# Kernel tuning notes

Hardware: AMD Instinct MI355X
Metric: run time of the kernel (lower is better)

Reference implementation:

```python
import jax, jax.numpy as jnp
import numpy as np

D_MODEL, D_FF, N_EXPERTS, TOP_K = 1024, 4096, 8, 2
BATCH, SEQ = 4, 2048


def setup_inputs() -> dict:
    key = jax.random.key(0)
    ks = jax.random.split(key, 8)
    s_in = 1.0 / np.sqrt(D_MODEL)
    s_ff = 1.0 / np.sqrt(D_FF)
    return {
        "x": jax.random.normal(ks[0], (BATCH, SEQ, D_MODEL), dtype=jnp.float32),
        "W_gate": jax.random.uniform(ks[1], (D_MODEL, N_EXPERTS), jnp.float32, -s_in, s_in),
        "b_gate": jax.random.uniform(ks[2], (N_EXPERTS,), jnp.float32, -s_in, s_in),
        "W1": jax.random.uniform(ks[3], (N_EXPERTS, D_MODEL, D_FF), jnp.float32, -s_in, s_in),
        "b1": jax.random.uniform(ks[4], (N_EXPERTS, D_FF), jnp.float32, -s_in, s_in),
        "W2": jax.random.uniform(ks[5], (N_EXPERTS, D_FF, D_MODEL), jnp.float32, -s_ff, s_ff),
        "b2": jax.random.uniform(ks[6], (N_EXPERTS, D_MODEL), jnp.float32, -s_ff, s_ff),
    }


def reference(x, W_gate, b_gate, W1, b1, W2, b2):
    B, S, D = x.shape
    # Router
    logits = jnp.einsum("bsd,de->bse", x, W_gate) + b_gate           # [B,S,E]
    probs = jax.nn.softmax(logits, axis=-1)
    top_p, top_i = jax.lax.top_k(probs, TOP_K)                        # [B,S,k]
    top_p = top_p / jnp.sum(top_p, axis=-1, keepdims=True)
    
    x_flat = x.reshape(-1, D)                                         # [T,D]
    idx_flat = top_i.reshape(-1, TOP_K)                               # [T,k]
    p_flat = top_p.reshape(-1, TOP_K)                                 # [T,k]
    
    # Dense all-expert FFN (faithful to original: every expert on every token)
    h = jax.nn.relu(jnp.einsum("td,edf->etf", x_flat, W1) + b1[:, None, :])  # [E,T,F]
    expert_out = jnp.einsum("etf,efd->etd", h, W2) + b2[:, None, :]          # [E,T,D]
    expert_out = jnp.transpose(expert_out, (1, 0, 2))                 # [T,E,D]
    
    # Gather top-k expert outputs and combine
    sel = jnp.take_along_axis(expert_out, idx_flat[:, :, None], axis=1)  # [T,k,D]
    out_flat = jnp.sum(sel * p_flat[:, :, None], axis=1)              # [T,D]
    output = out_flat.reshape(B, S, D)
    
    # torch.var defaults to unbiased (ddof=1)
    load_balance_loss = jnp.var(jnp.mean(probs, axis=(0, 1)), ddof=1)
    return (output, load_balance_loss)
```

## Files before the change

kernel.cpp:

```cpp
#include <hip/hip_runtime.h>
#include <cstdint>
#include <cstddef>

#define D_MODEL 1024
#define D_FF    4096
#define NEXP    8
#define NTOK    8192
#define MAXT    136
#define CAP     (MAXT * 128)

typedef unsigned short ushort_t;
typedef __attribute__((ext_vector_type(8))) short   short8;
typedef __attribute__((ext_vector_type(4))) float   floatx4;
typedef __attribute__((ext_vector_type(4))) unsigned short ushort4v;

__device__ __forceinline__ ushort_t f2bf(float f) {
    union { float f; uint32_t u; } v; v.f = f;
    uint32_t r = v.u + 0x7fffu + ((v.u >> 16) & 1u);
    return (ushort_t)(r >> 16);
}

__device__ __forceinline__ floatx4 mfma16(short8 a, short8 b, floatx4 c) {
    return __builtin_amdgcn_mfma_f32_16x16x32_bf16(a, b, c, 0, 0, 0);
}

__device__ __forceinline__ int tile_decode(const int* __restrict__ counts,
                                           int tm, int& e_out, int& row0) {
    int cnts[NEXP];
#pragma unroll
    for (int e = 0; e < NEXP; ++e) cnts[e] = counts[e];
    int b = 0, t = tm;
#pragma unroll
    for (int e = 0; e < NEXP; ++e) {
        int nt = (cnts[e] + 127) >> 7;
        if (t < nt) { e_out = e; row0 = b + t * 128; return 1; }
        t -= nt; b += nt * 128;
    }
    return 0;
}

__global__ __launch_bounds__(256)
void transpose_all(const float* __restrict__ W1, const float* __restrict__ W2,
                   ushort_t* __restrict__ W1T, ushort_t* __restrict__ W2T)
{
    __shared__ float t[64][65];
    int bid = blockIdx.x;
    const float* in; ushort_t* out; int R, C, rt, ct;
    if (bid < 8192) {
        int e = bid >> 10, rem = bid & 1023;
        R = D_MODEL; C = D_FF; rt = rem >> 6; ct = rem & 63;
        in = W1 + (size_t)e * R * C; out = W1T + (size_t)e * R * C;
    } else {
        int e = (bid - 8192) >> 10, rem = bid & 1023;
        R = D_FF; C = D_MODEL; rt = rem >> 4; ct = rem & 15;
        in = W2 + (size_t)e * R * C; out = W2T + (size_t)e * R * C;
    }
    int r0 = rt * 64, c0 = ct * 64, tid = threadIdx.x;
    int lr = tid >> 4, lc4 = (tid & 15) * 4;
#pragma unroll
    for (int p = 0; p < 4; ++p) {
        int rr = p * 16 + lr;
        float4 v = *(const float4*)(in + (size_t)(r0 + rr) * C + c0 + lc4);
        t[rr][lc4] = v.x; t[rr][lc4 + 1] = v.y; t[rr][lc4 + 2] = v.z; t[rr][lc4 + 3] = v.w;
    }
    __syncthreads();
    int orw = tid >> 3, j0 = (tid & 7) * 8;
#pragma unroll
    for (int p = 0; p < 2; ++p) {
        int orow = p * 32 + orw;
        ushort_t pk[8];
#pragma unroll
        for (int i = 0; i < 8; ++i) pk[i] = f2bf(t[j0 + i][orow]);
        *(short8*)(out + (size_t)(c0 + orow) * R + r0 + j0) = *(short8*)pk;
    }
}

__global__ __launch_bounds__(256)
void router_kernel(const float* __restrict__ x, const float* __restrict__ Wg,
                   const float* __restrict__ bg,
                   int* __restrict__ counts, int* __restrict__ slot_tok,
                   float* __restrict__ slot_p, float* __restrict__ psum)
{
    __shared__ float bsum[NEXP];
    int tid = threadIdx.x;
    if (tid < NEXP) bsum[tid] = 0.f;
    __syncthreads();

    int t = (blockIdx.x * 256 + tid) >> 6;
    int l = tid & 63;
    const float* xr = x + (size_t)t * D_MODEL;
    float acc[NEXP] = {0.f,0.f,0.f,0.f,0.f,0.f,0.f,0.f};
#pragma unroll 4
    for (int c = 0; c < D_MODEL / 64; ++c) {
        int d = c * 64 + l;
        float xv = xr[d];
        const float4* wr = (const float4*)(Wg + (size_t)d * NEXP);
        float4 w0 = wr[0], w1 = wr[1];
        acc[0] += xv * w0.x; acc[1] += xv * w0.y;
        acc[2] += xv * w0.z; acc[3] += xv * w0.w;
        acc[4] += xv * w1.x; acc[5] += xv * w1.y;
        acc[6] += xv * w1.z; acc[7] += xv * w1.w;
    }
#pragma unroll
    for (int off = 32; off >= 1; off >>= 1)
#pragma unroll
        for (int e = 0; e < NEXP; ++e)
            acc[e] += __shfl_xor(acc[e], off);

    if (l == 0) {
        float lg[NEXP], mx = -1e30f;
#pragma unroll
        for (int e = 0; e < NEXP; ++e) { lg[e] = acc[e] + bg[e]; mx = fmaxf(mx, lg[e]); }
        float pr[NEXP], s = 0.f;
#pragma unroll
        for (int e = 0; e < NEXP; ++e) { pr[e] = __expf(lg[e] - mx); s += pr[e]; }
        float inv = 1.f / s;
#pragma unroll
        for (int e = 0; e < NEXP; ++e) pr[e] *= inv;
        int e0 = 0;
#pragma unroll
        for (int e = 1; e < NEXP; ++e) if (pr[e] > pr[e0]) e0 = e;
        int e1 = (e0 == 0) ? 1 : 0;
#pragma unroll
        for (int e = 0; e < NEXP; ++e) if (e != e0 && pr[e] > pr[e1]) e1 = e;
        float pnorm = 1.f / (pr[e0] + pr[e1]);
        int s0 = atomicAdd(&counts[e0], 1);
        slot_tok[e0 * NTOK + s0] = t; slot_p[e0 * NTOK + s0] = pr[e0] * pnorm;
        int s1 = atomicAdd(&counts[e1], 1);
        slot_tok[e1 * NTOK + s1] = t; slot_p[e1 * NTOK + s1] = pr[e1] * pnorm;
#pragma unroll
        for (int e = 0; e < NEXP; ++e) atomicAdd(&bsum[e], pr[e]);
    }
    __syncthreads();
    if (tid < NEXP) atomicAdd(&psum[tid], bsum[tid]);
}

__global__ __launch_bounds__(256)
void gather_kernel(const float* __restrict__ x, const int* __restrict__ counts,
                   const int* __restrict__ slot_tok, const float* __restrict__ slot_p,
                   ushort_t* __restrict__ xg, float* __restrict__ tok_prob,
                   int* __restrict__ tcount, int* __restrict__ tok2row)
{
    __shared__ int sb[NEXP + 1];
    int row = blockIdx.x, tid = threadIdx.x;
    if (tid == 0) {
        int b = 0;
#pragma unroll
        for (int e = 0; e < NEXP; ++e) { sb[e] = b; b += ((counts[e] + 127) >> 7) << 7; }
        sb[NEXP] = b;
    }
    __syncthreads();
    if (row >= sb[NEXP]) return;
    int e = 0;
    while (e < NEXP - 1 && row >= sb[e + 1]) ++e;
    int lr = row - sb[e];
    int tok = -1; float pr = 0.f;
    if (lr < counts[e]) { tok = slot_tok[e * NTOK + lr]; pr = slot_p[e * NTOK + lr]; }
    if (tid == 0) {
        tok_prob[row] = pr;
        if (tok >= 0) {
            int s = atomicAdd(&tcount[tok], 1);
            tok2row[tok * 2 + s] = row;
        }
    }
    ushort_t* dst = xg + (size_t)row * D_MODEL;
    if (tok >= 0) {
        float4 v = ((const float4*)(x + (size_t)tok * D_MODEL))[tid];
        ushort4v o; o.x = f2bf(v.x); o.y = f2bf(v.y); o.z = f2bf(v.z); o.w = f2bf(v.w);
        *(ushort4v*)(dst + tid * 4) = o;
    } else {
        *(ushort4v*)(dst + tid * 4) = ushort4v{0, 0, 0, 0};
    }
}

template <int EPI>
__global__ __launch_bounds__(256, 2)
void gemm_tile(const ushort_t* __restrict__ A, const ushort_t* __restrict__ B,
               int K, int N, const int* __restrict__ counts,
               int row_lo, int row_hi,
               ushort_t* __restrict__ Hout, const float* __restrict__ bias,
               float* __restrict__ Yout)
{
    int NX = gridDim.x;
    int lin = blockIdx.y * NX + blockIdx.x;
    int sid = lin >> 4, wi = lin & 15;
    int nsx = NX >> 2;
    int sx = sid % nsx, sy = sid / nsx;
    int colbase = ((sx << 2) + (wi & 3)) * 128;
    int tm = (sy << 2) + (wi >> 2);

    int e, row0;
    if (!tile_decode(counts, tm, e, row0)) return;
    if (row0 < row_lo || row0 >= row_hi) return;

    __shared__ ushort_t smem[128 * 64 * 2];
    ushort_t* As = smem;
    ushort_t* Bs = smem + 128 * 64;

    int tid = threadIdx.x;
    int w = tid >> 6, l = tid & 63;
    int q = l >> 4, ml = l & 15;
    int wm = w >> 1, wn = w & 1;
    int r8 = l >> 3, ch = l & 7;

    const ushort_t* Ab = A + (size_t)row0 * K;
    const ushort_t* Bb = B + ((size_t)e * N + colbase) * K;

    floatx4 acc[4][4];
#pragma unroll
    for (int i = 0; i < 4; ++i)
#pragma unroll
        for (int j = 0; j < 4; ++j) acc[i][j] = floatx4{0.f, 0.f, 0.f, 0.f};

    short8 sa[4], sb[4];
    int rloc[4];
#pragma unroll
    for (int p = 0; p < 4; ++p) rloc[p] = (p * 4 + w) * 8 + r8;

#define GLOAD(k0)                                                          \
    do {                                                                   \
        _Pragma("unroll")                                                  \
        for (int p = 0; p < 4; ++p) {                                      \
            sa[p] = *(const short8*)(Ab + (size_t)rloc[p] * K + (k0) + ch * 8); \
            sb[p] = *(const short8*)(Bb + (size_t)rloc[p] * K + (k0) + ch * 8); \
        }                                                                  \
    } while (0)

    GLOAD(0);
    int nst = K >> 6;
    for (int s = 0; s < nst; ++s) {
#pragma unroll
        for (int p = 0; p < 4; ++p) {
            int r = rloc[p];
            int c = ch ^ r8;
            *(short8*)(As + r * 64 + c * 8) = sa[p];
            *(short8*)(Bs + r * 64 + c * 8) = sb[p];
        }
        __syncthreads();
        if (s + 1 < nst) GLOAD((s + 1) << 6);
#pragma unroll
        for (int kk = 0; kk < 2; ++kk) {
            int cb = kk * 4 + q;
            short8 av[4], bv[4];
#pragma unroll
            for (int mi = 0; mi < 4; ++mi) {
                int m = wm * 64 + mi * 16 + ml;
                av[mi] = *(const short8*)(As + m * 64 + ((cb ^ (m & 7)) * 8));
            }
#pragma unroll
            for (int ni = 0; ni < 4; ++ni) {
                int n = wn * 64 + ni * 16 + ml;
                bv[ni] = *(const short8*)(Bs + n * 64 + ((cb ^ (n & 7)) * 8));
            }
#pragma unroll
            for (int mi = 0; mi < 4; ++mi)
#pragma unroll
                for (int ni = 0; ni < 4; ++ni)
                    acc[mi][ni] = mfma16(av[mi], bv[ni], acc[mi][ni]);
        }
        __syncthreads();
    }
#undef GLOAD

    float bv4[4];
#pragma unroll
    for (int ni = 0; ni < 4; ++ni)
        bv4[ni] = bias[e * N + colbase + wn * 64 + ni * 16 + ml];

    if (EPI == 0) {
        ushort_t* ct = smem;
#pragma unroll
        for (int mi = 0; mi < 4; ++mi)
#pragma unroll
            for (int ni = 0; ni < 4; ++ni)
#pragma unroll
                for (int r = 0; r < 4; ++r) {
                    float v = acc[mi][ni][r] + bv4[ni];
                    v = v > 0.f ? v : 0.f;
                    ct[(wm * 64 + mi * 16 + q * 4 + r) * 128 + wn * 64 + ni * 16 + ml] = f2bf(v);
                }
        __syncthreads();
#pragma unroll
        for (int i = 0; i < 8; ++i) {
            int idx = tid + i * 256;
            int r = idx >> 4, c8 = idx & 15;
            *(short8*)(Hout + (size_t)(row0 + r) * D_FF + colbase + c8 * 8) =
                *(const short8*)(ct + r * 128 + c8 * 8);
        }
    } else {
#pragma unroll
        for (int mi = 0; mi < 4; ++mi)
#pragma unroll
            for (int ni = 0; ni < 4; ++ni)
#pragma unroll
                for (int r = 0; r < 4; ++r) {
                    int row = row0 + wm * 64 + mi * 16 + q * 4 + r;
                    int col = colbase + wn * 64 + ni * 16 + ml;
                    Yout[(size_t)row * N + col] = acc[mi][ni][r] + bv4[ni];
                }
    }
}

__global__ __launch_bounds__(256)
void combine_kernel(const float* __restrict__ y, const int* __restrict__ tok2row,
                    const float* __restrict__ tok_prob, float* __restrict__ out,
                    const float* __restrict__ psum, float* __restrict__ loss_out)
{
    int t = blockIdx.x;
    if (t == 0 && threadIdx.x == 0) {
        float me[NEXP], m = 0.f;
#pragma unroll
        for (int e = 0; e < NEXP; ++e) { me[e] = psum[e] * (1.f / NTOK); m += me[e] * (1.f / NEXP); }
        float v = 0.f;
#pragma unroll
        for (int e = 0; e < NEXP; ++e) v += (me[e] - m) * (me[e] - m);
        loss_out[0] = v * (1.f / (NEXP - 1));
    }
    int r0 = tok2row[t * 2], r1 = tok2row[t * 2 + 1];
    float p0 = tok_prob[r0], p1 = tok_prob[r1];
    int c = threadIdx.x;
    float4 a = ((const float4*)(y + (size_t)r0 * D_MODEL))[c];
    float4 b = ((const float4*)(y + (size_t)r1 * D_MODEL))[c];
    float4 o;
    o.x = p0 * a.x + p1 * b.x;
    o.y = p0 * a.y + p1 * b.y;
    o.z = p0 * a.z + p1 * b.z;
    o.w = p0 * a.w + p1 * b.w;
    ((float4*)(out + (size_t)t * D_MODEL))[c] = o;
}

extern "C" void kernel_launch(void* const* d_in, const int* in_sizes, int n_in,
                              void* d_out, int out_size, void* d_ws, size_t ws_size,
                              hipStream_t stream)
{
    const float* x  = (const float*)d_in[0];
    const float* Wg = (const float*)d_in[1];
    const float* bg = (const float*)d_in[2];
    const float* W1 = (const float*)d_in[3];
    const float* b1 = (const float*)d_in[4];
    const float* W2 = (const float*)d_in[5];
    const float* b2 = (const float*)d_in[6];
    float* out = (float*)d_out;

    char* ws = (char*)d_ws;
    size_t off = 0;
    auto alloc = [&](size_t bytes) -> char* {
        char* p = ws + off;
        off = (off + bytes + 255) & ~(size_t)255;
        return p;
    };
    int*      counts   = (int*)alloc(NEXP * 4);
    float*    psum     = (float*)alloc(NEXP * 4);
    int*      tcount   = (int*)alloc(NTOK * 4);
    size_t zero_bytes = off;
    float*    tok_prob = (float*)alloc(CAP * 4);
    int*      tok2row  = (int*)alloc((size_t)NTOK * 2 * 4);
    int*      slot_tok = (int*)alloc((size_t)NEXP * NTOK * 4);
    float*    slot_p   = (float*)alloc((size_t)NEXP * NTOK * 4);
    ushort_t* xg       = (ushort_t*)alloc((size_t)CAP * D_MODEL * 2);
    ushort_t* W1T      = (ushort_t*)alloc((size_t)NEXP * D_MODEL * D_FF * 2);
    ushort_t* W2T      = (ushort_t*)alloc((size_t)NEXP * D_MODEL * D_FF * 2);
    float*    ybuf     = (float*)alloc((size_t)CAP * D_MODEL * 4);
    size_t fixed = off;
    size_t h_full = (size_t)CAP * D_FF * 2;

    int NC = 1;
    if (ws_size < fixed + h_full) NC = 4;
    if (NC == 4 && ws_size < fixed + h_full / 4) NC = 16;
    if (ws_size < fixed + h_full / NC) return;
    int chunk_rows = CAP / NC;
    ushort_t* hbuf = (ushort_t*)alloc(h_full / NC);

    hipMemsetAsync(d_ws, 0, zero_bytes, stream);

    transpose_all<<<16384, 256, 0, stream>>>(W1, W2, W1T, W2T);
    router_kernel<<<NTOK / 4, 256, 0, stream>>>(x, Wg, bg, counts, slot_tok, slot_p, psum);
    gather_kernel<<<CAP, 256, 0, stream>>>(x, counts, slot_tok, slot_p, xg,
                                           tok_prob, tcount, tok2row);
    for (int c = 0; c < NC; ++c) {
        int lo = c * chunk_rows, hi = lo + chunk_rows;
        ushort_t* h_eff = hbuf - (ptrdiff_t)lo * D_FF;
        gemm_tile<0><<<dim3(D_FF / 128, MAXT), 256, 0, stream>>>(
            xg, W1T, D_MODEL, D_FF, counts, lo, hi, h_eff, b1, nullptr);
        gemm_tile<1><<<dim3(D_MODEL / 128, MAXT), 256, 0, stream>>>(
            h_eff, W2T, D_FF, D_MODEL, counts, lo, hi, nullptr, b2, ybuf);
    }
    combine_kernel<<<NTOK, 256, 0, stream>>>(ybuf, tok2row, tok_prob, out, psum,
                                             out + (size_t)out_size - 1);
    (void)in_sizes; (void)n_in;
}
```

Before: 881.8 us.

## Load GEMM tiles directly to LDS and remap workgroups across XCDs

Replaces the register-staged global-to-LDS copy with global_load_lds direct transfers, applying the XOR swizzle to the global source address. This drops the VGPR staging and the separate LDS writes. It also remaps the linear workgroup index so consecutive tiles land on the same XCD, which should improve L2 reuse. The change loses the software prefetch of the next K-slice, so loads are no longer overlapped with MFMA compute within a single block. Correctness of the remap assumes the workgroup count is divisible by 8.

```diff
diff --git a/kernel.cpp b/kernel.cpp
--- a/kernel.cpp
+++ b/kernel.cpp
@@ -22,6 +22,12 @@
 
 __device__ __forceinline__ floatx4 mfma16(short8 a, short8 b, floatx4 c) {
     return __builtin_amdgcn_mfma_f32_16x16x32_bf16(a, b, c, 0, 0, 0);
+}
+
+__device__ __forceinline__ void gload16(const ushort_t* g, ushort_t* l) {
+    __builtin_amdgcn_global_load_lds(
+        (const __attribute__((address_space(1))) void*)g,
+        (__attribute__((address_space(3))) void*)l, 16, 0, 0);
 }
 
 __device__ __forceinline__ int tile_decode(const int* __restrict__ counts,
@@ -182,7 +188,10 @@
                float* __restrict__ Yout)
 {
     int NX = gridDim.x;
-    int lin = blockIdx.y * NX + blockIdx.x;
+    int nwg = NX * (int)gridDim.y;
+    int lin0 = blockIdx.y * NX + blockIdx.x;
+    int cpx = nwg >> 3;
+    int lin = (lin0 & 7) * cpx + (lin0 >> 3);
     int sid = lin >> 4, wi = lin & 15;
     int nsx = NX >> 2;
     int sx = sid % nsx, sy = sid / nsx;
@@ -201,43 +210,37 @@
     int w = tid >> 6, l = tid & 63;
     int q = l >> 4, ml = l & 15;
     int wm = w >> 1, wn = w & 1;
-    int r8 = l >> 3, ch = l & 7;
 
     const ushort_t* Ab = A + (size_t)row0 * K;
     const ushort_t* Bb = B + ((size_t)e * N + colbase) * K;
 
+    const ushort_t* ag[4]; const ushort_t* bg[4];
+    ushort_t* al[4]; ushort_t* bl[4];
+#pragma unroll
+    for (int i = 0; i < 4; ++i) {
+        int rr = (i * 4 + w) * 8 + (l >> 3);
+        int cc = ((l & 7) ^ (rr & 7)) * 8;
+        ag[i] = Ab + (size_t)rr * K + cc;
+        bg[i] = Bb + (size_t)rr * K + cc;
+        al[i] = As + (i * 4 + w) * 512;
+        bl[i] = Bs + (i * 4 + w) * 512;
+    }
+
     floatx4 acc[4][4];
 #pragma unroll
     for (int i = 0; i < 4; ++i)
 #pragma unroll
         for (int j = 0; j < 4; ++j) acc[i][j] = floatx4{0.f, 0.f, 0.f, 0.f};
 
-    short8 sa[4], sb[4];
-    int rloc[4];
-#pragma unroll
-    for (int p = 0; p < 4; ++p) rloc[p] = (p * 4 + w) * 8 + r8;
-
-#define GLOAD(k0)                                                          \
-    do {                                                                   \
-        _Pragma("unroll")                                                  \
-        for (int p = 0; p < 4; ++p) {                                      \
-            sa[p] = *(const short8*)(Ab + (size_t)rloc[p] * K + (k0) + ch * 8); \
-            sb[p] = *(const short8*)(Bb + (size_t)rloc[p] * K + (k0) + ch * 8); \
-        }                                                                  \
-    } while (0)
-
-    GLOAD(0);
     int nst = K >> 6;
     for (int s = 0; s < nst; ++s) {
 #pragma unroll
-        for (int p = 0; p < 4; ++p) {
-            int r = rloc[p];
-            int c = ch ^ r8;
-            *(short8*)(As + r * 64 + c * 8) = sa[p];
-            *(short8*)(Bs + r * 64 + c * 8) = sb[p];
+        for (int i = 0; i < 4; ++i) {
+            gload16(ag[i], al[i]);
+            gload16(bg[i], bl[i]);
+            ag[i] += 64; bg[i] += 64;
         }
         __syncthreads();
-        if (s + 1 < nst) GLOAD((s + 1) << 6);
 #pragma unroll
         for (int kk = 0; kk < 2; ++kk) {
             int cb = kk * 4 + q;
@@ -260,7 +263,6 @@
         }
         __syncthreads();
     }
-#undef GLOAD
 
     float bv4[4];
 #pragma unroll
```

After: 881.0 us. About the same (-0.1%).
